# Optimization experiments

Measured on AMD Instinct MI355X. Metric: run time of the kernel, lower is better.

The kernel has to match this reference:

```python
import jax, jax.numpy as jnp
import numpy as np

EMBED_DIM = 1024
NUM_HEADS = 16
HEAD_DIM = EMBED_DIM // NUM_HEADS
SCALE = HEAD_DIM ** -0.5


def setup_inputs() -> dict:
    key = jax.random.key(0)
    ks = jax.random.split(key, 11)
    B, T, C = 4, 2048, EMBED_DIM
    s = 1.0 / np.sqrt(C)
    return {
        "query": jax.random.normal(ks[0], (B, T, C), jnp.float32),
        "key": jax.random.normal(ks[1], (B, T, C), jnp.float32),
        "value": jax.random.normal(ks[2], (B, T, C), jnp.float32),
        "Wq": jax.random.normal(ks[3], (C, C), jnp.float32) * s,
        "bq": jnp.zeros((C,), jnp.float32),
        "Wk": jax.random.normal(ks[4], (C, C), jnp.float32) * s,
        "bk": jnp.zeros((C,), jnp.float32),
        "Wv": jax.random.normal(ks[5], (C, C), jnp.float32) * s,
        "bv": jnp.zeros((C,), jnp.float32),
        "Wo": jax.random.normal(ks[6], (C, C), jnp.float32) * s,
        "bo": jnp.zeros((C,), jnp.float32),
    }


def reference(query, key, value, Wq, bq, Wk, bk, Wv, bv, Wo, bo):
    B, Tq, C = query.shape
    Tk = key.shape[1]
    H, D = NUM_HEADS, HEAD_DIM
    # Linear projections (torch Linear: x @ W.T + b), split heads -> (B, H, T, D)
    q = (query @ Wq.T + bq).reshape(B, Tq, H, D).transpose(0, 2, 1, 3)
    k = (key @ Wk.T + bk).reshape(B, Tk, H, D).transpose(0, 2, 1, 3)
    v = (value @ Wv.T + bv).reshape(B, Tk, H, D).transpose(0, 2, 1, 3)
    scores = jnp.einsum("bhqd,bhkd->bhqk", q, k) * SCALE
    attn = jax.nn.softmax(scores, axis=-1)
    out = jnp.einsum("bhqk,bhkd->bhqd", attn, v)
    out = out.transpose(0, 2, 1, 3).reshape(B, Tq, C)
    return out @ Wo.T + bo
```

## Files before the change

kernel.cpp:

```cpp
#include <hip/hip_runtime.h>
#include <stdint.h>
#include <math.h>

#define C_DIM 1024
#define H_NUM 16
#define D_DIM 64
#define B_NUM 4
#define T_SEQ 2048
#define M_ROWS (B_NUM * T_SEQ)

#define SCALE_LOG2E (0.125f * 1.44269504088896340736f)

typedef __attribute__((ext_vector_type(8))) __bf16 bf16x8;
typedef __attribute__((ext_vector_type(2))) __bf16 bf16x2;
typedef __attribute__((ext_vector_type(4))) float f32x4;

__device__ __forceinline__ unsigned short f2bf(float f) {
  union { float f; uint32_t u; } v; v.f = f;
  uint32_t r = v.u + 0x7FFFu + ((v.u >> 16) & 1u);
  return (unsigned short)(r >> 16);
}

__device__ __forceinline__ uint32_t pk2bf(float a, float b) {
#if __has_builtin(__builtin_amdgcn_cvt_pk_bf16_f32)
  union { bf16x2 v; uint32_t u; } u;
  u.v = __builtin_amdgcn_cvt_pk_bf16_f32(a, b);
  return u.u;
#else
  union { float f; uint32_t u; } x, y; x.f = a; y.f = b;
  return __builtin_amdgcn_perm(y.u + 0x8000u, x.u + 0x8000u, 0x07060302u);
#endif
}

__device__ __forceinline__ float frcp(float x) {
#if __has_builtin(__builtin_amdgcn_rcpf)
  return __builtin_amdgcn_rcpf(x);
#else
  return 1.f / x;
#endif
}

__device__ __forceinline__ f32x4 mfma16(bf16x8 a, bf16x8 b, f32x4 c) {
  return __builtin_amdgcn_mfma_f32_16x16x32_bf16(a, b, c, 0, 0, 0);
}

__device__ __forceinline__ void cp16(const void* g, void* l) {
  __builtin_amdgcn_global_load_lds(
      (const __attribute__((address_space(1))) unsigned int*)g,
      (__attribute__((address_space(3))) unsigned int*)l, 16, 0, 0);
}

__global__ __launch_bounds__(256) void cast3(
    const float* __restrict__ a, const float* __restrict__ b,
    const float* __restrict__ c, unsigned short* __restrict__ oa,
    unsigned short* __restrict__ ob, unsigned short* __restrict__ oc, int n4) {
  int i = blockIdx.x * 256 + threadIdx.x;
  if (i >= n4) return;
  const float* s = (blockIdx.y == 0) ? a : (blockIdx.y == 1) ? b : c;
  unsigned short* d = (blockIdx.y == 0) ? oa : (blockIdx.y == 1) ? ob : oc;
  float4 v = ((const float4*)s)[i];
  ushort4 o;
  o.x = f2bf(v.x); o.y = f2bf(v.y); o.z = f2bf(v.z); o.w = f2bf(v.w);
  ((ushort4*)d)[i] = o;
}

__global__ __launch_bounds__(256) void cast4(
    const float* __restrict__ a, const float* __restrict__ b,
    const float* __restrict__ c, const float* __restrict__ e,
    unsigned short* __restrict__ oa, unsigned short* __restrict__ ob,
    unsigned short* __restrict__ oc, unsigned short* __restrict__ oe, int n4) {
  int i = blockIdx.x * 256 + threadIdx.x;
  if (i >= n4) return;
  const float* s = (blockIdx.y == 0) ? a : (blockIdx.y == 1) ? b
                   : (blockIdx.y == 2) ? c : e;
  unsigned short* d = (blockIdx.y == 0) ? oa : (blockIdx.y == 1) ? ob
                      : (blockIdx.y == 2) ? oc : oe;
  float4 v = ((const float4*)s)[i];
  ushort4 o;
  o.x = f2bf(v.x); o.y = f2bf(v.y); o.z = f2bf(v.z); o.w = f2bf(v.w);
  ((ushort4*)d)[i] = o;
}

__device__ __forceinline__ void gemm_tile_128(
    const unsigned short* __restrict__ A, const unsigned short* __restrict__ Bw,
    int row0, int col0, unsigned short* As, unsigned short* Bs, f32x4 acc[4][4]) {
  const int lane = threadIdx.x & 63;
  const int wave = threadIdx.x >> 6;
  const int wm = wave >> 1, wn = wave & 1;
#pragma unroll
  for (int mt = 0; mt < 4; ++mt)
#pragma unroll
    for (int nt = 0; nt < 4; ++nt) acc[mt][nt] = (f32x4){0.f, 0.f, 0.f, 0.f};

  for (int k0 = 0; k0 < C_DIM; k0 += 64) {
    __syncthreads();
#pragma unroll
    for (int rr = 0; rr < 4; ++rr) {
      int c = (rr * 4 + wave) * 64 + lane;
      int row = c >> 3;
      int g = (c & 7) ^ (row & 7);
      cp16(A + (size_t)(row0 + row) * C_DIM + k0 + g * 8, As + (rr * 4 + wave) * 512);
      cp16(Bw + (size_t)(col0 + row) * C_DIM + k0 + g * 8, Bs + (rr * 4 + wave) * 512);
    }
    __syncthreads();
#pragma unroll
    for (int ks = 0; ks < 2; ++ks) {
      bf16x8 af[4], bfr[4];
#pragma unroll
      for (int mt = 0; mt < 4; ++mt) {
        int row = wm * 64 + mt * 16 + (lane & 15);
        int gs = (ks * 4 + (lane >> 4)) ^ (row & 7);
        af[mt] = *(const bf16x8*)(As + row * 64 + gs * 8);
      }
#pragma unroll
      for (int nt = 0; nt < 4; ++nt) {
        int row = wn * 64 + nt * 16 + (lane & 15);
        int gs = (ks * 4 + (lane >> 4)) ^ (row & 7);
        bfr[nt] = *(const bf16x8*)(Bs + row * 64 + gs * 8);
      }
#pragma unroll
      for (int mt = 0; mt < 4; ++mt)
#pragma unroll
        for (int nt = 0; nt < 4; ++nt)
          acc[mt][nt] = mfma16(af[mt], bfr[nt], acc[mt][nt]);
    }
  }
}

__global__ __launch_bounds__(256) void gemm_qkv(
    const unsigned short* __restrict__ qb, const unsigned short* __restrict__ kb,
    const unsigned short* __restrict__ vb, const unsigned short* __restrict__ wq,
    const unsigned short* __restrict__ wk, const unsigned short* __restrict__ wv,
    const float* __restrict__ bq, const float* __restrict__ bk,
    const float* __restrict__ bv, unsigned short* __restrict__ Qp,
    unsigned short* __restrict__ Kp, unsigned short* __restrict__ Vp) {
  __shared__ alignas(16) unsigned short As[128 * 64];
  __shared__ alignas(16) unsigned short Bs[128 * 64];
  const int z = blockIdx.z;
  const unsigned short* A = (z == 0) ? qb : (z == 1) ? kb : vb;
  const unsigned short* W = (z == 0) ? wq : (z == 1) ? wk : wv;
  const float* bias = (z == 0) ? bq : (z == 1) ? bk : bv;
  const int row0 = blockIdx.y * 128, col0 = blockIdx.x * 128;
  f32x4 acc[4][4];
  gemm_tile_128(A, W, row0, col0, As, Bs, acc);

  const int lane = threadIdx.x & 63;
  const int wave = threadIdx.x >> 6;
  const int wm = wave >> 1, wn = wave & 1;
  const int quad = lane >> 4;
#pragma unroll
  for (int mt = 0; mt < 4; ++mt)
#pragma unroll
    for (int nt = 0; nt < 4; ++nt) {
      int n = col0 + wn * 64 + nt * 16 + (lane & 15);
      float bval = bias[n];
      int h = n >> 6, d = n & 63;
      if (z == 2) {
        int m0 = row0 + wm * 64 + mt * 16 + quad * 4;
        int b = m0 >> 11, t0 = m0 & 2047;
        float f0 = acc[mt][nt][0] + bval, f1 = acc[mt][nt][1] + bval;
        float f2 = acc[mt][nt][2] + bval, f3 = acc[mt][nt][3] + bval;
        uint2 pk = {pk2bf(f0, f1), pk2bf(f2, f3)};
        size_t off = (((size_t)(b * H_NUM + h) * (T_SEQ / 8) + (t0 >> 3)) * D_DIM + d) * 8
                     + (t0 & 7);
        *(uint2*)(Vp + off) = pk;
      } else {
#pragma unroll
        for (int r = 0; r < 4; ++r) {
          int m = row0 + wm * 64 + mt * 16 + quad * 4 + r;
          int b = m >> 11, t = m & 2047;
          float f = acc[mt][nt][r] + bval;
          if (z == 0) f *= SCALE_LOG2E;
          unsigned short val = f2bf(f);
          if (z == 0)
            Qp[((size_t)(b * H_NUM + h) * T_SEQ + t) * D_DIM + d] = val;
          else
            Kp[((size_t)(b * H_NUM + h) * T_SEQ + t) * D_DIM + d] = val;
        }
      }
    }
}

__global__ __launch_bounds__(128, 2) void attn_kernel(
    const unsigned short* __restrict__ Qp, const unsigned short* __restrict__ Kp,
    const unsigned short* __restrict__ Vp, unsigned short* __restrict__ Op) {
  __shared__ alignas(16) unsigned short Ks[64 * 64];
  __shared__ alignas(16) unsigned short Vt[8 * 64 * 8];
  __shared__ alignas(16) unsigned short Pw[2][4][16 * 72];
  const int bh = blockIdx.y;
  const int q0 = blockIdx.x * 128;
  const int lane = threadIdx.x & 63;
  const int wave = threadIdx.x >> 6;
  const int quad = lane >> 4;
  const int q15 = lane & 15;

  bf16x8 qf[4][2];
#pragma unroll
  for (int g = 0; g < 4; ++g) {
    const unsigned short* qrow =
        Qp + ((size_t)bh * T_SEQ + q0 + wave * 64 + g * 16 + q15) * D_DIM;
    qf[g][0] = *(const bf16x8*)(qrow + quad * 8);
    qf[g][1] = *(const bf16x8*)(qrow + 32 + quad * 8);
  }

  bf16x8 onesf;
#pragma unroll
  for (int i = 0; i < 8; ++i) onesf[i] = (__bf16)1.0f;

  f32x4 oacc[4][4];
  f32x4 lacc[4];
#pragma unroll
  for (int g = 0; g < 4; ++g) {
    lacc[g] = (f32x4){0.f, 0.f, 0.f, 0.f};
#pragma unroll
    for (int dt = 0; dt < 4; ++dt) oacc[g][dt] = (f32x4){0.f, 0.f, 0.f, 0.f};
  }

  const unsigned short* Kbase = Kp + (size_t)bh * T_SEQ * D_DIM;
  const unsigned short* Vbase = Vp + (size_t)bh * T_SEQ * D_DIM;

  for (int kt = 0; kt < T_SEQ / 64; ++kt) {
    __syncthreads();
#pragma unroll
    for (int rr = 0; rr < 4; ++rr) {
      int c = (rr * 2 + wave) * 64 + lane;
      int krow = c >> 3;
      int kg = (c & 7) ^ (krow & 7);
      cp16(Kbase + ((size_t)(kt * 64 + krow)) * D_DIM + kg * 8,
           Ks + (rr * 2 + wave) * 512);
      cp16(Vbase + (size_t)(kt * 8 + (rr * 2 + wave)) * 512 + lane * 8,
           Vt + (rr * 2 + wave) * 512);
    }
    __syncthreads();

    bf16x8 kfr[4][2];
#pragma unroll
    for (int mt = 0; mt < 4; ++mt) {
      int row = mt * 16 + q15;
#pragma unroll
      for (int ks = 0; ks < 2; ++ks) {
        int gs = (ks * 4 + quad) ^ (row & 7);
        kfr[mt][ks] = *(const bf16x8*)(Ks + row * 64 + gs * 8);
      }
    }
#pragma unroll
    for (int g = 0; g < 4; ++g) {
      f32x4 s[4];
#pragma unroll
      for (int mt = 0; mt < 4; ++mt) s[mt] = (f32x4){0.f, 0.f, 0.f, 0.f};
#pragma unroll
      for (int ks = 0; ks < 2; ++ks)
#pragma unroll
        for (int mt = 0; mt < 4; ++mt)
          s[mt] = mfma16(kfr[mt][ks], qf[g][ks], s[mt]);
      unsigned short* Pg = &Pw[wave][g][0];
#pragma unroll
      for (int mt = 0; mt < 4; ++mt) {
        float p0 = __builtin_amdgcn_exp2f(s[mt][0]);
        float p1 = __builtin_amdgcn_exp2f(s[mt][1]);
        float p2 = __builtin_amdgcn_exp2f(s[mt][2]);
        float p3 = __builtin_amdgcn_exp2f(s[mt][3]);
        uint2 pk = {pk2bf(p0, p1), pk2bf(p2, p3)};
        *(uint2*)(Pg + q15 * 72 + mt * 16 + quad * 4) = pk;
      }
    }
    __builtin_amdgcn_s_waitcnt(0xC07F);

    bf16x8 vfr[4][2];
#pragma unroll
    for (int dt = 0; dt < 4; ++dt)
#pragma unroll
      for (int ks = 0; ks < 2; ++ks)
        vfr[dt][ks] = *(const bf16x8*)(Vt + (ks * 4 + quad) * 512 + (dt * 16 + q15) * 8);
#pragma unroll
    for (int g = 0; g < 4; ++g) {
      const unsigned short* Pg = &Pw[wave][g][0];
      bf16x8 pf0 = *(const bf16x8*)(Pg + q15 * 72 + quad * 8);
      bf16x8 pf1 = *(const bf16x8*)(Pg + q15 * 72 + (4 + quad) * 8);
      lacc[g] = mfma16(pf0, onesf, lacc[g]);
      lacc[g] = mfma16(pf1, onesf, lacc[g]);
#pragma unroll
      for (int dt = 0; dt < 4; ++dt) {
        oacc[g][dt] = mfma16(pf0, vfr[dt][0], oacc[g][dt]);
        oacc[g][dt] = mfma16(pf1, vfr[dt][1], oacc[g][dt]);
      }
    }
  }

  const int b = bh >> 4, h = bh & 15;
#pragma unroll
  for (int g = 0; g < 4; ++g) {
    float inv[4];
#pragma unroll
    for (int r = 0; r < 4; ++r) inv[r] = frcp(lacc[g][r]);
#pragma unroll
    for (int dt = 0; dt < 4; ++dt)
#pragma unroll
      for (int r = 0; r < 4; ++r) {
        int t = q0 + wave * 64 + g * 16 + quad * 4 + r;
        int col = h * D_DIM + dt * 16 + q15;
        Op[((size_t)b * T_SEQ + t) * C_DIM + col] = f2bf(oacc[g][dt][r] * inv[r]);
      }
  }
}

__global__ __launch_bounds__(256) void gemm_out_kernel(
    const unsigned short* __restrict__ Op, const unsigned short* __restrict__ wo,
    const float* __restrict__ bo, float* __restrict__ out) {
  __shared__ alignas(16) unsigned short As[128 * 64];
  __shared__ alignas(16) unsigned short Bs[128 * 64];
  const int row0 = blockIdx.y * 128, col0 = blockIdx.x * 128;
  f32x4 acc[4][4];
  gemm_tile_128(Op, wo, row0, col0, As, Bs, acc);

  const int lane = threadIdx.x & 63;
  const int wave = threadIdx.x >> 6;
  const int wm = wave >> 1, wn = wave & 1;
#pragma unroll
  for (int mt = 0; mt < 4; ++mt)
#pragma unroll
    for (int nt = 0; nt < 4; ++nt) {
      int n = col0 + wn * 64 + nt * 16 + (lane & 15);
      float bval = bo[n];
#pragma unroll
      for (int r = 0; r < 4; ++r) {
        int m = row0 + wm * 64 + mt * 16 + (lane >> 4) * 4 + r;
        out[(size_t)m * C_DIM + n] = acc[mt][nt][r] + bval;
      }
    }
}

extern "C" void kernel_launch(void* const* d_in, const int* in_sizes, int n_in,
                              void* d_out, int out_size, void* d_ws, size_t ws_size,
                              hipStream_t stream) {
  const float* q_in = (const float*)d_in[0];
  const float* k_in = (const float*)d_in[1];
  const float* v_in = (const float*)d_in[2];
  const float* Wq = (const float*)d_in[3];
  const float* bq = (const float*)d_in[4];
  const float* Wk = (const float*)d_in[5];
  const float* bk = (const float*)d_in[6];
  const float* Wv = (const float*)d_in[7];
  const float* bv = (const float*)d_in[8];
  const float* Wo = (const float*)d_in[9];
  const float* bo = (const float*)d_in[10];
  float* out = (float*)d_out;

  const size_t MC = (size_t)M_ROWS * C_DIM;
  const size_t CC = (size_t)C_DIM * C_DIM;
  unsigned short* qb = (unsigned short*)d_ws;
  unsigned short* kb = qb + MC;
  unsigned short* vb = kb + MC;
  unsigned short* wqb = vb + MC;
  unsigned short* wkb = wqb + CC;
  unsigned short* wvb = wkb + CC;
  unsigned short* wob = wvb + CC;
  unsigned short* Qp = wob + CC;
  unsigned short* Kp = Qp + MC;
  unsigned short* Vp = Kp + MC;
  unsigned short* Op = Vp + MC;

  const int big4 = (int)(MC / 4), small4 = (int)(CC / 4);
  cast3<<<dim3((big4 + 255) / 256, 3), dim3(256), 0, stream>>>(
      q_in, k_in, v_in, qb, kb, vb, big4);
  cast4<<<dim3((small4 + 255) / 256, 4), dim3(256), 0, stream>>>(
      Wq, Wk, Wv, Wo, wqb, wkb, wvb, wob, small4);

  gemm_qkv<<<dim3(C_DIM / 128, M_ROWS / 128, 3), dim3(256), 0, stream>>>(
      qb, kb, vb, wqb, wkb, wvb, bq, bk, bv, Qp, Kp, Vp);

  attn_kernel<<<dim3(T_SEQ / 128, B_NUM * H_NUM), dim3(128), 0, stream>>>(
      Qp, Kp, Vp, Op);

  gemm_out_kernel<<<dim3(C_DIM / 128, M_ROWS / 128), dim3(256), 0, stream>>>(
      Op, wob, bo, out);
}
```

Baseline: 346.5 us.

## Double-buffer attention K/V tiles, keep P in registers, merge cast kernels

The attention kernel now uses 256 threads with 32 queries per wave and double-buffers the K and V tiles in LDS. The next tile is prefetched while the current one is computed, which removes one barrier per iteration. The score MFMA operand order is swapped so the bf16 probability fragments stay in registers, which drops the LDS round trip for P and its waitcnt. K rows are permuted with a new swizzle, output stores are vectorised, the grid order puts heads on the x dimension, and the two cast kernels are merged into one launch. The risks are higher register pressure at a 3-block occupancy target, and many idle blocks for the weight rows of the merged cast, whose grid is sized for the large tensors.

```diff
diff --git a/kernel.cpp b/kernel.cpp
--- a/kernel.cpp
+++ b/kernel.cpp
@@ -50,31 +50,30 @@
       (__attribute__((address_space(3))) unsigned int*)l, 16, 0, 0);
 }
 
-__global__ __launch_bounds__(256) void cast3(
-    const float* __restrict__ a, const float* __restrict__ b,
-    const float* __restrict__ c, unsigned short* __restrict__ oa,
-    unsigned short* __restrict__ ob, unsigned short* __restrict__ oc, int n4) {
+__global__ __launch_bounds__(256) void cast_all(
+    const float* __restrict__ a0, const float* __restrict__ a1,
+    const float* __restrict__ a2, const float* __restrict__ w0,
+    const float* __restrict__ w1, const float* __restrict__ w2,
+    const float* __restrict__ w3, unsigned short* __restrict__ oa0,
+    unsigned short* __restrict__ oa1, unsigned short* __restrict__ oa2,
+    unsigned short* __restrict__ ow0, unsigned short* __restrict__ ow1,
+    unsigned short* __restrict__ ow2, unsigned short* __restrict__ ow3,
+    int big4, int small4) {
   int i = blockIdx.x * 256 + threadIdx.x;
+  int y = blockIdx.y;
+  const float* s;
+  unsigned short* d;
+  int n4;
+  switch (y) {
+    case 0: s = a0; d = oa0; n4 = big4; break;
+    case 1: s = a1; d = oa1; n4 = big4; break;
+    case 2: s = a2; d = oa2; n4 = big4; break;
+    case 3: s = w0; d = ow0; n4 = small4; break;
+    case 4: s = w1; d = ow1; n4 = small4; break;
+    case 5: s = w2; d = ow2; n4 = small4; break;
+    default: s = w3; d = ow3; n4 = small4; break;
+  }
   if (i >= n4) return;
-  const float* s = (blockIdx.y == 0) ? a : (blockIdx.y == 1) ? b : c;
-  unsigned short* d = (blockIdx.y == 0) ? oa : (blockIdx.y == 1) ? ob : oc;
-  float4 v = ((const float4*)s)[i];
-  ushort4 o;
-  o.x = f2bf(v.x); o.y = f2bf(v.y); o.z = f2bf(v.z); o.w = f2bf(v.w);
-  ((ushort4*)d)[i] = o;
-}
-
-__global__ __launch_bounds__(256) void cast4(
-    const float* __restrict__ a, const float* __restrict__ b,
-    const float* __restrict__ c, const float* __restrict__ e,
-    unsigned short* __restrict__ oa, unsigned short* __restrict__ ob,
-    unsigned short* __restrict__ oc, unsigned short* __restrict__ oe, int n4) {
-  int i = blockIdx.x * 256 + threadIdx.x;
-  if (i >= n4) return;
-  const float* s = (blockIdx.y == 0) ? a : (blockIdx.y == 1) ? b
-                   : (blockIdx.y == 2) ? c : e;
-  unsigned short* d = (blockIdx.y == 0) ? oa : (blockIdx.y == 1) ? ob
-                      : (blockIdx.y == 2) ? oc : oe;
   float4 v = ((const float4*)s)[i];
   ushort4 o;
   o.x = f2bf(v.x); o.y = f2bf(v.y); o.z = f2bf(v.z); o.w = f2bf(v.w);
@@ -181,24 +180,25 @@
     }
 }
 
-__global__ __launch_bounds__(128, 2) void attn_kernel(
+__device__ __forceinline__ int fsw(int r) { return (r + ((r >> 3) << 2)) & 7; }
+
+__global__ __launch_bounds__(256, 3) void attn_kernel(
     const unsigned short* __restrict__ Qp, const unsigned short* __restrict__ Kp,
     const unsigned short* __restrict__ Vp, unsigned short* __restrict__ Op) {
-  __shared__ alignas(16) unsigned short Ks[64 * 64];
-  __shared__ alignas(16) unsigned short Vt[8 * 64 * 8];
-  __shared__ alignas(16) unsigned short Pw[2][4][16 * 72];
-  const int bh = blockIdx.y;
-  const int q0 = blockIdx.x * 128;
+  __shared__ alignas(16) unsigned short Ks[2][64 * 64];
+  __shared__ alignas(16) unsigned short Vt[2][64 * 64];
+  const int bh = blockIdx.x;
+  const int q0 = blockIdx.y * 128;
   const int lane = threadIdx.x & 63;
   const int wave = threadIdx.x >> 6;
   const int quad = lane >> 4;
   const int q15 = lane & 15;
 
-  bf16x8 qf[4][2];
-#pragma unroll
-  for (int g = 0; g < 4; ++g) {
+  bf16x8 qf[2][2];
+#pragma unroll
+  for (int g = 0; g < 2; ++g) {
     const unsigned short* qrow =
-        Qp + ((size_t)bh * T_SEQ + q0 + wave * 64 + g * 16 + q15) * D_DIM;
+        Qp + ((size_t)bh * T_SEQ + q0 + wave * 32 + g * 16 + q15) * D_DIM;
     qf[g][0] = *(const bf16x8*)(qrow + quad * 8);
     qf[g][1] = *(const bf16x8*)(qrow + 32 + quad * 8);
   }
@@ -207,10 +207,10 @@
 #pragma unroll
   for (int i = 0; i < 8; ++i) onesf[i] = (__bf16)1.0f;
 
-  f32x4 oacc[4][4];
-  f32x4 lacc[4];
-#pragma unroll
-  for (int g = 0; g < 4; ++g) {
+  f32x4 oacc[2][4];
+  f32x4 lacc[2];
+#pragma unroll
+  for (int g = 0; g < 2; ++g) {
     lacc[g] = (f32x4){0.f, 0.f, 0.f, 0.f};
 #pragma unroll
     for (int dt = 0; dt < 4; ++dt) oacc[g][dt] = (f32x4){0.f, 0.f, 0.f, 0.f};
@@ -219,32 +219,40 @@
   const unsigned short* Kbase = Kp + (size_t)bh * T_SEQ * D_DIM;
   const unsigned short* Vbase = Vp + (size_t)bh * T_SEQ * D_DIM;
 
+#define STAGE(kt, buf)                                                        \
+  {                                                                           \
+    _Pragma("unroll") for (int i = 0; i < 2; ++i) {                           \
+      int chunk = wave * 2 + i;                                     \
+      int c = chunk * 64 + lane;                                              \
+      int row = c >> 3;                                                       \
+      int g = (c & 7) ^ fsw(row);                                             \
+      cp16(Kbase + ((size_t)((kt) * 64 + row)) * D_DIM + g * 8,               \
+           &Ks[buf][chunk * 512]);                                            \
+      cp16(Vbase + (size_t)((kt) * 8 + chunk) * 512 + lane * 8,               \
+           &Vt[buf][chunk * 512]);                                            \
+    }                                                                         \
+  }
+
+  STAGE(0, 0);
+
   for (int kt = 0; kt < T_SEQ / 64; ++kt) {
+    const int buf = kt & 1;
     __syncthreads();
-#pragma unroll
-    for (int rr = 0; rr < 4; ++rr) {
-      int c = (rr * 2 + wave) * 64 + lane;
-      int krow = c >> 3;
-      int kg = (c & 7) ^ (krow & 7);
-      cp16(Kbase + ((size_t)(kt * 64 + krow)) * D_DIM + kg * 8,
-           Ks + (rr * 2 + wave) * 512);
-      cp16(Vbase + (size_t)(kt * 8 + (rr * 2 + wave)) * 512 + lane * 8,
-           Vt + (rr * 2 + wave) * 512);
-    }
-    __syncthreads();
+    if (kt + 1 < T_SEQ / 64) STAGE(kt + 1, buf ^ 1);
 
     bf16x8 kfr[4][2];
 #pragma unroll
     for (int mt = 0; mt < 4; ++mt) {
-      int row = mt * 16 + q15;
+      int rowp = 32 * (mt >> 1) + (q15 >> 2) * 8 + (mt & 1) * 4 + (q15 & 3);
 #pragma unroll
       for (int ks = 0; ks < 2; ++ks) {
-        int gs = (ks * 4 + quad) ^ (row & 7);
-        kfr[mt][ks] = *(const bf16x8*)(Ks + row * 64 + gs * 8);
-      }
-    }
-#pragma unroll
-    for (int g = 0; g < 4; ++g) {
+        int gs = (ks * 4 + quad) ^ fsw(rowp);
+        kfr[mt][ks] = *(const bf16x8*)(&Ks[buf][rowp * 64 + gs * 8]);
+      }
+    }
+    bf16x8 Pb[2][2];
+#pragma unroll
+    for (int g = 0; g < 2; ++g) {
       f32x4 s[4];
 #pragma unroll
       for (int mt = 0; mt < 4; ++mt) s[mt] = (f32x4){0.f, 0.f, 0.f, 0.f};
@@ -253,54 +261,52 @@
 #pragma unroll
         for (int mt = 0; mt < 4; ++mt)
           s[mt] = mfma16(kfr[mt][ks], qf[g][ks], s[mt]);
-      unsigned short* Pg = &Pw[wave][g][0];
-#pragma unroll
-      for (int mt = 0; mt < 4; ++mt) {
-        float p0 = __builtin_amdgcn_exp2f(s[mt][0]);
-        float p1 = __builtin_amdgcn_exp2f(s[mt][1]);
-        float p2 = __builtin_amdgcn_exp2f(s[mt][2]);
-        float p3 = __builtin_amdgcn_exp2f(s[mt][3]);
-        uint2 pk = {pk2bf(p0, p1), pk2bf(p2, p3)};
-        *(uint2*)(Pg + q15 * 72 + mt * 16 + quad * 4) = pk;
-      }
-    }
-    __builtin_amdgcn_s_waitcnt(0xC07F);
-
-    bf16x8 vfr[4][2];
-#pragma unroll
-    for (int dt = 0; dt < 4; ++dt)
-#pragma unroll
-      for (int ks = 0; ks < 2; ++ks)
-        vfr[dt][ks] = *(const bf16x8*)(Vt + (ks * 4 + quad) * 512 + (dt * 16 + q15) * 8);
-#pragma unroll
-    for (int g = 0; g < 4; ++g) {
-      const unsigned short* Pg = &Pw[wave][g][0];
-      bf16x8 pf0 = *(const bf16x8*)(Pg + q15 * 72 + quad * 8);
-      bf16x8 pf1 = *(const bf16x8*)(Pg + q15 * 72 + (4 + quad) * 8);
-      lacc[g] = mfma16(pf0, onesf, lacc[g]);
-      lacc[g] = mfma16(pf1, onesf, lacc[g]);
+#pragma unroll
+      for (int a = 0; a < 2; ++a) {
+        float p0 = __builtin_amdgcn_exp2f(s[2 * a][0]);
+        float p1 = __builtin_amdgcn_exp2f(s[2 * a][1]);
+        float p2 = __builtin_amdgcn_exp2f(s[2 * a][2]);
+        float p3 = __builtin_amdgcn_exp2f(s[2 * a][3]);
+        float p4 = __builtin_amdgcn_exp2f(s[2 * a + 1][0]);
+        float p5 = __builtin_amdgcn_exp2f(s[2 * a + 1][1]);
+        float p6 = __builtin_amdgcn_exp2f(s[2 * a + 1][2]);
+        float p7 = __builtin_amdgcn_exp2f(s[2 * a + 1][3]);
+        union { bf16x8 v; uint32_t u[4]; } pk;
+        pk.u[0] = pk2bf(p0, p1);
+        pk.u[1] = pk2bf(p2, p3);
+        pk.u[2] = pk2bf(p4, p5);
+        pk.u[3] = pk2bf(p6, p7);
+        Pb[g][a] = pk.v;
+      }
+    }
+
+#pragma unroll
+    for (int a = 0; a < 2; ++a) {
+      lacc[0] = mfma16(onesf, Pb[0][a], lacc[0]);
+      lacc[1] = mfma16(onesf, Pb[1][a], lacc[1]);
 #pragma unroll
       for (int dt = 0; dt < 4; ++dt) {
-        oacc[g][dt] = mfma16(pf0, vfr[dt][0], oacc[g][dt]);
-        oacc[g][dt] = mfma16(pf1, vfr[dt][1], oacc[g][dt]);
-      }
-    }
-  }
+        bf16x8 vf =
+            *(const bf16x8*)(&Vt[buf][((a * 4 + quad) * 64 + dt * 16 + q15) * 8]);
+        oacc[0][dt] = mfma16(vf, Pb[0][a], oacc[0][dt]);
+        oacc[1][dt] = mfma16(vf, Pb[1][a], oacc[1][dt]);
+      }
+    }
+  }
+#undef STAGE
 
   const int b = bh >> 4, h = bh & 15;
 #pragma unroll
-  for (int g = 0; g < 4; ++g) {
-    float inv[4];
-#pragma unroll
-    for (int r = 0; r < 4; ++r) inv[r] = frcp(lacc[g][r]);
-#pragma unroll
-    for (int dt = 0; dt < 4; ++dt)
-#pragma unroll
-      for (int r = 0; r < 4; ++r) {
-        int t = q0 + wave * 64 + g * 16 + quad * 4 + r;
-        int col = h * D_DIM + dt * 16 + q15;
-        Op[((size_t)b * T_SEQ + t) * C_DIM + col] = f2bf(oacc[g][dt][r] * inv[r]);
-      }
+  for (int g = 0; g < 2; ++g) {
+    float inv = frcp(lacc[g][0]);
+    int t = q0 + wave * 32 + g * 16 + q15;
+#pragma unroll
+    for (int dt = 0; dt < 4; ++dt) {
+      uint2 o = {pk2bf(oacc[g][dt][0] * inv, oacc[g][dt][1] * inv),
+                 pk2bf(oacc[g][dt][2] * inv, oacc[g][dt][3] * inv)};
+      int col = h * D_DIM + dt * 16 + quad * 4;
+      *(uint2*)(Op + ((size_t)b * T_SEQ + t) * C_DIM + col) = o;
+    }
   }
 }
 
@@ -361,15 +367,14 @@
   unsigned short* Op = Vp + MC;
 
   const int big4 = (int)(MC / 4), small4 = (int)(CC / 4);
-  cast3<<<dim3((big4 + 255) / 256, 3), dim3(256), 0, stream>>>(
-      q_in, k_in, v_in, qb, kb, vb, big4);
-  cast4<<<dim3((small4 + 255) / 256, 4), dim3(256), 0, stream>>>(
-      Wq, Wk, Wv, Wo, wqb, wkb, wvb, wob, small4);
+  cast_all<<<dim3((big4 + 255) / 256, 7), dim3(256), 0, stream>>>(
+      q_in, k_in, v_in, Wq, Wk, Wv, Wo, qb, kb, vb, wqb, wkb, wvb, wob,
+      big4, small4);
 
   gemm_qkv<<<dim3(C_DIM / 128, M_ROWS / 128, 3), dim3(256), 0, stream>>>(
       qb, kb, vb, wqb, wkb, wvb, bq, bk, bv, Qp, Kp, Vp);
 
-  attn_kernel<<<dim3(T_SEQ / 128, B_NUM * H_NUM), dim3(128), 0, stream>>>(
+  attn_kernel<<<dim3(B_NUM * H_NUM, T_SEQ / 128), dim3(256), 0, stream>>>(
       Qp, Kp, Vp, Op);
 
   gemm_out_kernel<<<dim3(C_DIM / 128, M_ROWS / 128), dim3(256), 0, stream>>>(
```

New measurement: 334.3 us. 1.04x faster.
